# Optimization experiments

Hardware: AMD Instinct MI355X
Metric: run time of the kernel (lower is better)

## Reference

```python
import jax, jax.numpy as jnp
import numpy as np

N_NODES = 50000
N_EDGES = 800000
D_IN = 128
D_HID = 128
D_OUT = 128
EPS = 0.1  # GINConv eps


def setup_inputs() -> dict:
    key = jax.random.key(0)
    k = jax.random.split(key, 8)
    scale = 1.0 / np.sqrt(D_IN)
    return {
        "x": jax.random.normal(k[0], (N_NODES, D_IN), dtype=jnp.float32),
        "edge_index": jax.random.randint(k[1], (2, N_EDGES), 0, N_NODES, dtype=jnp.int64),
        "edge_weight": jax.random.uniform(k[2], (N_EDGES,), dtype=jnp.float32),
        "W1a": jax.random.normal(k[3], (D_IN, D_HID), dtype=jnp.float32) * scale,
        "W1b": jax.random.normal(k[4], (D_HID, D_HID), dtype=jnpp.float32) if False else jax.random.normal(k[4], (D_HID, D_HID), dtype=jnp.float32) * scale,
        "W2a": jax.random.normal(k[5], (D_HID, D_HID), dtype=jnp.float32) * scale,
        "W2b": jax.random.normal(k[6], (D_HID, D_OUT), dtype=jnp.float32) * scale,
    }


def _gin_conv(h, src, dst, ew, Wa, Wb, n_nodes):
    # edge-weighted neighbor sum: aggr[i] = sum_{(j->i)} w_ji * h[j]
    msg = ew[:, None] * h[src]                       # [E, d]
    aggr = jax.ops.segment_sum(msg, dst, num_segments=n_nodes)  # [N, d]
    z = (1.0 + EPS) * h + aggr                       # GIN update
    # 2-layer bias-free MLP: lin -> relu -> lin
    return jnp.maximum(z @ Wa, 0.0) @ Wb


def reference(x, edge_index, edge_weight, W1a, W1b, W2a, W2b):
    src, dst = edge_index[0], edge_index[1]
    n = x.shape[0]
    h = _gin_conv(x, src, dst, edge_weight, W1a, W1b, n)
    h = jnp.maximum(h, 0.0)  # relu between convs; dropout is identity in eval
    h = _gin_conv(h, src, dst, edge_weight, W2a, W2b, n)
    return h
```

## Files before the change

kernel.cpp:

```cpp
#include <hip/hip_runtime.h>
#include <hip/hip_fp16.h>

#define D 128
#define N_NODES 50000
#define EPSP1 1.1f

#define NPB 256
#define NBUCK 196
#define CAP 5120
#define P1E 2048
#define TS 136

typedef __attribute__((ext_vector_type(8))) short short8;
typedef __attribute__((ext_vector_type(4))) float f32x4;

__device__ __forceinline__ unsigned short f2bf(float f) {
    unsigned u = __float_as_uint(f);
    u += 0x7FFF + ((u >> 16) & 1);
    return (unsigned short)(u >> 16);
}
__device__ __forceinline__ float bf2f(unsigned short h) {
    return __uint_as_float(((unsigned)h) << 16);
}

__global__ __launch_bounds__(256) void fused_pre(
    const int* __restrict__ src, const int* __restrict__ dst,
    const float* __restrict__ ew, int* __restrict__ gcnt,
    uint2* __restrict__ gstage, int ne,
    const float* __restrict__ x, unsigned short* __restrict__ hb, int n4,
    const float* __restrict__ W1a, const float* __restrict__ W1b,
    const float* __restrict__ W2a, const float* __restrict__ W2b,
    unsigned short* __restrict__ wp, int p1grid, int cgrid)
{
    int bid = blockIdx.x;
    int tid = threadIdx.x;
    if (bid < p1grid) {
        __shared__ int bcnt[NBUCK];
        __shared__ int goff[NBUCK];
        if (tid < NBUCK) bcnt[tid] = 0;
        __syncthreads();
        int e0 = bid * P1E;
        int   rank[8];
        int   buck[8];
        uint2 pay[8];
#pragma unroll
        for (int j = 0; j < 8; ++j) {
            int e = e0 + j * 256 + tid;
            buck[j] = -1;
            if (e < ne) {
                int d_ = dst[e];
                int b  = d_ >> 8;
                int dl = d_ & 255;
                pay[j].x = (unsigned)(src[e] & 0xFFFF) | ((unsigned)dl << 16);
                pay[j].y = (unsigned)__half_as_ushort(__float2half_rn(ew[e]));
                rank[j]  = atomicAdd(&bcnt[b], 1);
                buck[j]  = b;
            }
        }
        __syncthreads();
        if (tid < NBUCK && bcnt[tid] > 0)
            goff[tid] = atomicAdd(&gcnt[tid], bcnt[tid]);
        __syncthreads();
#pragma unroll
        for (int j = 0; j < 8; ++j) {
            if (buck[j] >= 0) {
                int pos = goff[buck[j]] + rank[j];
                if (pos < CAP)
                    gstage[(size_t)buck[j] * CAP + pos] = pay[j];
            }
        }
    } else if (bid < p1grid + cgrid) {
        int base = (bid - p1grid) * 1024;
#pragma unroll
        for (int it = 0; it < 4; ++it) {
            int i = base + it * 256 + tid;
            if (i < n4) {
                float4 v = ((const float4*)x)[i];
                ushort4 o;
                o.x = f2bf(v.x); o.y = f2bf(v.y); o.z = f2bf(v.z); o.w = f2bf(v.w);
                ((ushort4*)hb)[i] = o;
            }
        }
    } else {
        int pb = bid - p1grid - cgrid;
        int mat = pb >> 3;
        const float* W = (mat == 0) ? W1a : (mat == 1) ? W1b : (mat == 2) ? W2a : W2b;
        unsigned short* Wp = wp + (size_t)mat * 16384;
        int e = (pb & 7) * 256 + tid;
        int col = e & 127;
        int kq  = e >> 7;
        short8 v;
#pragma unroll
        for (int j = 0; j < 8; ++j)
            v[j] = (short)f2bf(W[(size_t)(kq * 8 + j) * 128 + col]);
        ((short8*)Wp)[e] = v;
    }
}

__global__ __launch_bounds__(512) void csr_build(
    const uint2* __restrict__ gstage, const int* __restrict__ gcnt,
    unsigned* __restrict__ epay, int* __restrict__ off)
{
    __shared__ int hist[NPB];
    __shared__ int scan[NPB];
    __shared__ int bscan[NPB];
    __shared__ int loc[NPB];
    __shared__ unsigned csr[CAP];

    int b = blockIdx.x;
    int t = threadIdx.x;
    int cnt = min(gcnt[b], CAP);

    if (t < NPB) hist[t] = 0;
    __syncthreads();

    uint2 ent[CAP / 512];
#pragma unroll
    for (int it = 0; it < CAP / 512; ++it) {
        int i = it * 512 + t;
        if (i < cnt) {
            ent[it] = gstage[(size_t)b * CAP + i];
            atomicAdd(&hist[(ent[it].x >> 16) & 255], 1);
        }
    }
    __syncthreads();

    if (t < NPB) {
        scan[t]  = hist[t];
        bscan[t] = (t < b) ? min(gcnt[t], CAP) : 0;
    }
    __syncthreads();
    for (int dd = 1; dd < NPB; dd <<= 1) {
        int a0 = 0, a1 = 0;
        if (t < NPB && t >= dd) { a0 = scan[t - dd]; a1 = bscan[t - dd]; }
        __syncthreads();
        if (t < NPB && t >= dd) { scan[t] += a0; bscan[t] += a1; }
        __syncthreads();
    }
    int base = bscan[NPB - 1];

    if (t < NPB) {
        int node = (b << 8) + t;
        int excl = scan[t] - hist[t];
        if (node <= N_NODES) off[node] = base + excl;
        loc[t] = excl;
    }
    __syncthreads();

#pragma unroll
    for (int it = 0; it < CAP / 512; ++it) {
        int i = it * 512 + t;
        if (i < cnt) {
            int dl = (ent[it].x >> 16) & 255;
            int p = atomicAdd(&loc[dl], 1);
            csr[p] = (ent[it].x & 0xFFFF) | (ent[it].y << 16);
        }
    }
    __syncthreads();

    for (int i = t; i < cnt; i += 512)
        epay[base + i] = csr[i];
}

__global__ __launch_bounds__(256) void gather_kernel(
    const unsigned short* __restrict__ h, const int* __restrict__ off,
    const unsigned* __restrict__ epay, unsigned short* __restrict__ z, int n_nodes)
{
    int tid = threadIdx.x;
    int node = blockIdx.x * 4 + (tid >> 6);
    if (node >= n_nodes) return;
    int lane = tid & 63;
    int qtr  = lane >> 4;
    int sub  = lane & 15;
    int beg = off[node];
    int end = off[node + 1];
    float acc[8];
#pragma unroll
    for (int c = 0; c < 8; ++c) acc[c] = 0.f;

    int i = beg;
    for (; i + 8 <= end; i += 8) {
        unsigned p0 = epay[i + qtr];
        unsigned p1 = epay[i + 4 + qtr];
        short8 v0 = ((const short8*)(h + (size_t)(p0 & 0xFFFF) * D))[sub];
        short8 v1 = ((const short8*)(h + (size_t)(p1 & 0xFFFF) * D))[sub];
        float w0 = __half2float(__ushort_as_half((unsigned short)(p0 >> 16)));
        float w1 = __half2float(__ushort_as_half((unsigned short)(p1 >> 16)));
#pragma unroll
        for (int c = 0; c < 8; ++c)
            acc[c] += w0 * bf2f((unsigned short)v0[c]) + w1 * bf2f((unsigned short)v1[c]);
    }
    for (; i + qtr < end; i += 4) {
        unsigned p0 = epay[i + qtr];
        short8 v0 = ((const short8*)(h + (size_t)(p0 & 0xFFFF) * D))[sub];
        float w0 = __half2float(__ushort_as_half((unsigned short)(p0 >> 16)));
#pragma unroll
        for (int c = 0; c < 8; ++c)
            acc[c] += w0 * bf2f((unsigned short)v0[c]);
    }

#pragma unroll
    for (int c = 0; c < 8; ++c) {
        acc[c] += __shfl(acc[c], (lane + 32) & 63, 64);
        acc[c] += __shfl(acc[c], (lane + 16) & 63, 64);
    }

    if (qtr == 0) {
        short8 xv = ((const short8*)(h + (size_t)node * D))[sub];
        short8 o;
#pragma unroll
        for (int c = 0; c < 8; ++c) {
            float v = acc[c] + EPSP1 * bf2f((unsigned short)xv[c]);
            o[c] = (short)f2bf(v);
        }
        ((short8*)(z + (size_t)node * D))[sub] = o;
    }
}

template<int RELU2, int OUT_F32>
__global__ __launch_bounds__(256) void mlp_fused(
    const unsigned short* __restrict__ A,
    const unsigned short* __restrict__ WpA,
    const unsigned short* __restrict__ WpB,
    void* __restrict__ outv, int n)
{
    __shared__ unsigned short t[128 * TS];

    int tid  = threadIdx.x;
    int wave = tid >> 6;
    int lane = tid & 63;
    int quad = lane >> 4;
    int lc   = lane & 15;
    int rbase = blockIdx.x * 128 + wave * 32;
    int rloc  = wave * 32;

    const short8 zero8 = {0, 0, 0, 0, 0, 0, 0, 0};

    short8 a[2][4];
#pragma unroll
    for (int s = 0; s < 2; ++s) {
        int row = rbase + s * 16 + lc;
        const unsigned short* ap = A + (size_t)row * D;
#pragma unroll
        for (int kk = 0; kk < 4; ++kk)
            a[s][kk] = (row < n) ? *(const short8*)(ap + kk * 32 + quad * 8) : zero8;
    }

    f32x4 acc[2][8];
#pragma unroll
    for (int s = 0; s < 2; ++s)
#pragma unroll
        for (int c = 0; c < 8; ++c)
            acc[s][c] = (f32x4){0.f, 0.f, 0.f, 0.f};

#pragma unroll
    for (int cf = 0; cf < 8; ++cf) {
        short8 b[4];
#pragma unroll
        for (int kk = 0; kk < 4; ++kk)
            b[kk] = *(const short8*)(WpA + ((size_t)(kk * 4 + quad) * 128 + cf * 16 + lc) * 8);
#pragma unroll
        for (int kk = 0; kk < 4; ++kk) {
            acc[0][cf] = __builtin_amdgcn_mfma_f32_16x16x32_bf16(a[0][kk], b[kk], acc[0][cf], 0, 0, 0);
            acc[1][cf] = __builtin_amdgcn_mfma_f32_16x16x32_bf16(a[1][kk], b[kk], acc[1][cf], 0, 0, 0);
        }
    }

#pragma unroll
    for (int s = 0; s < 2; ++s)
#pragma unroll
        for (int reg = 0; reg < 4; ++reg) {
            int row = rloc + s * 16 + quad * 4 + reg;
#pragma unroll
            for (int cf = 0; cf < 8; ++cf)
                t[row * TS + cf * 16 + lc] = f2bf(fmaxf(acc[s][cf][reg], 0.f));
        }
    __syncthreads();

#pragma unroll
    for (int s = 0; s < 2; ++s) {
        int row = rloc + s * 16 + lc;
#pragma unroll
        for (int kk = 0; kk < 4; ++kk)
            a[s][kk] = *(const short8*)&t[row * TS + kk * 32 + quad * 8];
    }
#pragma unroll
    for (int s = 0; s < 2; ++s)
#pragma unroll
        for (int c = 0; c < 8; ++c)
            acc[s][c] = (f32x4){0.f, 0.f, 0.f, 0.f};

#pragma unroll
    for (int cf = 0; cf < 8; ++cf) {
        short8 b[4];
#pragma unroll
        for (int kk = 0; kk < 4; ++kk)
            b[kk] = *(const short8*)(WpB + ((size_t)(kk * 4 + quad) * 128 + cf * 16 + lc) * 8);
#pragma unroll
        for (int kk = 0; kk < 4; ++kk) {
            acc[0][cf] = __builtin_amdgcn_mfma_f32_16x16x32_bf16(a[0][kk], b[kk], acc[0][cf], 0, 0, 0);
            acc[1][cf] = __builtin_amdgcn_mfma_f32_16x16x32_bf16(a[1][kk], b[kk], acc[1][cf], 0, 0, 0);
        }
    }

#pragma unroll
    for (int s = 0; s < 2; ++s)
#pragma unroll
        for (int reg = 0; reg < 4; ++reg) {
            int row = rbase + s * 16 + quad * 4 + reg;
            if (row < n) {
#pragma unroll
                for (int cf = 0; cf < 8; ++cf) {
                    float v = acc[s][cf][reg];
                    if (RELU2) v = fmaxf(v, 0.f);
                    int col = cf * 16 + lc;
                    if (OUT_F32)
                        ((float*)outv)[(size_t)row * D + col] = v;
                    else
                        ((unsigned short*)outv)[(size_t)row * D + col] = f2bf(v);
                }
            }
        }
}

extern "C" void kernel_launch(void* const* d_in, const int* in_sizes, int n_in,
                              void* d_out, int out_size, void* d_ws, size_t ws_size,
                              hipStream_t stream) {
    const float* x   = (const float*)d_in[0];
    const int*   ei  = (const int*)d_in[1];
    const float* ew  = (const float*)d_in[2];
    const float* W1a = (const float*)d_in[3];
    const float* W1b = (const float*)d_in[4];
    const float* W2a = (const float*)d_in[5];
    const float* W2b = (const float*)d_in[6];
    float* out = (float*)d_out;

    int n_edges = in_sizes[2];
    const int* src = ei;
    const int* dst = ei + n_edges;

    size_t node_elems = (size_t)N_NODES * D;
    unsigned short* hb = (unsigned short*)d_ws;
    unsigned short* zb = hb + node_elems;
    unsigned short* wp = zb + node_elems;
    unsigned* epay = (unsigned*)(wp + 4 * 16384);
    uint2*  gstage = (uint2*)(epay + n_edges);
    int*    gcnt   = (int*)(gstage + (size_t)NBUCK * CAP);
    int*    off    = gcnt + NBUCK;

    int p1grid = (n_edges + P1E - 1) / P1E;
    int cgrid  = ((int)(node_elems / 4) + 1023) / 1024;
    int ggrid  = (N_NODES + 127) / 128;
    int agrid  = (N_NODES + 3) / 4;

    hipMemsetAsync(gcnt, 0, NBUCK * sizeof(int), stream);

    fused_pre<<<p1grid + cgrid + 32, 256, 0, stream>>>(
        src, dst, ew, gcnt, gstage, n_edges,
        x, hb, (int)(node_elems / 4),
        W1a, W1b, W2a, W2b, wp, p1grid, cgrid);

    csr_build<<<NBUCK, 512, 0, stream>>>(gstage, gcnt, epay, off);

    unsigned short* wp0 = wp;
    unsigned short* wp1 = wp + 16384;
    unsigned short* wp2 = wp + 2 * 16384;
    unsigned short* wp3 = wp + 3 * 16384;

    gather_kernel<<<agrid, 256, 0, stream>>>(hb, off, epay, zb, N_NODES);
    mlp_fused<1, 0><<<ggrid, 256, 0, stream>>>(zb, wp0, wp1, hb, N_NODES);

    gather_kernel<<<agrid, 256, 0, stream>>>(hb, off, epay, zb, N_NODES);
    mlp_fused<0, 1><<<ggrid, 256, 0, stream>>>(zb, wp2, wp3, out, N_NODES);
}
```

Before: 201.5 us.

## Move conversions into CSR build kernel, use wave-shuffle scans, unroll gather by 16

Splits edge bucketing into its own kernel and fuses the x and weight bf16 conversions into the CSR-build launch, so the CSR blocks run alongside the conversion blocks instead of the bucketing blocks. The 256-wide shared-memory Hillis-Steele scan with many barriers is replaced by wave-level shuffle scans plus a single-wave reduction for the bucket base offset. The gather loop gains a 16-edge unrolled stage to keep more loads in flight. The grid size hardcodes 782 conversion blocks, which ties the kernel to this node count.

```diff
diff --git a/kernel.cpp b/kernel.cpp
--- a/kernel.cpp
+++ b/kernel.cpp
@@ -23,57 +23,135 @@
     return __uint_as_float(((unsigned)h) << 16);
 }
 
-__global__ __launch_bounds__(256) void fused_pre(
+__global__ __launch_bounds__(256) void pass1_bucket(
     const int* __restrict__ src, const int* __restrict__ dst,
     const float* __restrict__ ew, int* __restrict__ gcnt,
-    uint2* __restrict__ gstage, int ne,
+    uint2* __restrict__ gstage, int ne)
+{
+    __shared__ int bcnt[NBUCK];
+    __shared__ int goff[NBUCK];
+    int tid = threadIdx.x;
+    int bid = blockIdx.x;
+    if (tid < NBUCK) bcnt[tid] = 0;
+    __syncthreads();
+    int e0 = bid * P1E;
+    int   rank[8];
+    int   buck[8];
+    uint2 pay[8];
+#pragma unroll
+    for (int j = 0; j < 8; ++j) {
+        int e = e0 + j * 256 + tid;
+        buck[j] = -1;
+        if (e < ne) {
+            int d_ = dst[e];
+            int b  = d_ >> 8;
+            int dl = d_ & 255;
+            pay[j].x = (unsigned)(src[e] & 0xFFFF) | ((unsigned)dl << 16);
+            pay[j].y = (unsigned)__half_as_ushort(__float2half_rn(ew[e]));
+            rank[j]  = atomicAdd(&bcnt[b], 1);
+            buck[j]  = b;
+        }
+    }
+    __syncthreads();
+    if (tid < NBUCK && bcnt[tid] > 0)
+        goff[tid] = atomicAdd(&gcnt[tid], bcnt[tid]);
+    __syncthreads();
+#pragma unroll
+    for (int j = 0; j < 8; ++j) {
+        if (buck[j] >= 0) {
+            int pos = goff[buck[j]] + rank[j];
+            if (pos < CAP)
+                gstage[(size_t)buck[j] * CAP + pos] = pay[j];
+        }
+    }
+}
+
+__global__ __launch_bounds__(512) void fused_mid(
+    const uint2* __restrict__ gstage, const int* __restrict__ gcnt,
+    unsigned* __restrict__ epay, int* __restrict__ off,
     const float* __restrict__ x, unsigned short* __restrict__ hb, int n4,
     const float* __restrict__ W1a, const float* __restrict__ W1b,
     const float* __restrict__ W2a, const float* __restrict__ W2b,
-    unsigned short* __restrict__ wp, int p1grid, int cgrid)
+    unsigned short* __restrict__ wp)
 {
+    __shared__ int hist[NPB];
+    __shared__ int scn[NPB];
+    __shared__ int loc[NPB];
+    __shared__ int wtot[8];
+    __shared__ int base_s;
+    __shared__ unsigned csr[CAP];
+
     int bid = blockIdx.x;
-    int tid = threadIdx.x;
-    if (bid < p1grid) {
-        __shared__ int bcnt[NBUCK];
-        __shared__ int goff[NBUCK];
-        if (tid < NBUCK) bcnt[tid] = 0;
+    int t = threadIdx.x;
+
+    if (bid < NBUCK) {
+        int b = bid;
+        int cnt = min(gcnt[b], CAP);
+
+        if (t < NPB) hist[t] = 0;
         __syncthreads();
-        int e0 = bid * P1E;
-        int   rank[8];
-        int   buck[8];
-        uint2 pay[8];
-#pragma unroll
-        for (int j = 0; j < 8; ++j) {
-            int e = e0 + j * 256 + tid;
-            buck[j] = -1;
-            if (e < ne) {
-                int d_ = dst[e];
-                int b  = d_ >> 8;
-                int dl = d_ & 255;
-                pay[j].x = (unsigned)(src[e] & 0xFFFF) | ((unsigned)dl << 16);
-                pay[j].y = (unsigned)__half_as_ushort(__float2half_rn(ew[e]));
-                rank[j]  = atomicAdd(&bcnt[b], 1);
-                buck[j]  = b;
+
+        uint2 ent[CAP / 512];
+#pragma unroll
+        for (int it = 0; it < CAP / 512; ++it) {
+            int i = it * 512 + t;
+            if (i < cnt) {
+                ent[it] = gstage[(size_t)b * CAP + i];
+                atomicAdd(&hist[(ent[it].x >> 16) & 255], 1);
             }
         }
         __syncthreads();
-        if (tid < NBUCK && bcnt[tid] > 0)
-            goff[tid] = atomicAdd(&gcnt[tid], bcnt[tid]);
+
+        int w = t >> 6, l = t & 63;
+        if (w < 4) {
+            int v = hist[w * 64 + l];
+#pragma unroll
+            for (int dd = 1; dd < 64; dd <<= 1) {
+                int u = __shfl_up(v, dd, 64);
+                if (l >= dd) v += u;
+            }
+            scn[w * 64 + l] = v;
+            if (l == 63) wtot[w] = v;
+        } else if (w == 4) {
+            int v = 0;
+            for (int i = l; i < NBUCK; i += 64)
+                if (i < b) v += min(gcnt[i], CAP);
+#pragma unroll
+            for (int dd = 32; dd > 0; dd >>= 1) v += __shfl_down(v, dd, 64);
+            if (l == 0) base_s = v;
+        }
         __syncthreads();
-#pragma unroll
-        for (int j = 0; j < 8; ++j) {
-            if (buck[j] >= 0) {
-                int pos = goff[buck[j]] + rank[j];
-                if (pos < CAP)
-                    gstage[(size_t)buck[j] * CAP + pos] = pay[j];
+
+        if (t < NPB) {
+            int pre = 0;
+#pragma unroll
+            for (int j = 0; j < 3; ++j) if (j < w) pre += wtot[j];
+            int incl = scn[t] + pre;
+            int excl = incl - hist[t];
+            int node = (b << 8) + t;
+            if (node <= N_NODES) off[node] = base_s + excl;
+            loc[t] = excl;
+        }
+        __syncthreads();
+
+#pragma unroll
+        for (int it = 0; it < CAP / 512; ++it) {
+            int i = it * 512 + t;
+            if (i < cnt) {
+                int dl = (ent[it].x >> 16) & 255;
+                int p = atomicAdd(&loc[dl], 1);
+                csr[p] = (ent[it].x & 0xFFFF) | (ent[it].y << 16);
             }
         }
-    } else if (bid < p1grid + cgrid) {
-        int base = (bid - p1grid) * 1024;
+        __syncthreads();
+
+        for (int i = t; i < cnt; i += 512)
+            epay[base_s + i] = csr[i];
+    } else if (bid < NBUCK + 782) {
+        int base = (bid - NBUCK) * 2048;
 #pragma unroll
         for (int it = 0; it < 4; ++it) {
-            int i = base + it * 256 + tid;
+            int i = base + it * 512 + t;
             if (i < n4) {
                 float4 v = ((const float4*)x)[i];
                 ushort4 o;
@@ -82,11 +160,11 @@
             }
         }
     } else {
-        int pb = bid - p1grid - cgrid;
-        int mat = pb >> 3;
+        int e2 = (bid - NBUCK - 782) * 512 + t;
+        int mat = e2 >> 11;
+        int e   = e2 & 2047;
         const float* W = (mat == 0) ? W1a : (mat == 1) ? W1b : (mat == 2) ? W2a : W2b;
         unsigned short* Wp = wp + (size_t)mat * 16384;
-        int e = (pb & 7) * 256 + tid;
         int col = e & 127;
         int kq  = e >> 7;
         short8 v;
@@ -95,71 +173,6 @@
             v[j] = (short)f2bf(W[(size_t)(kq * 8 + j) * 128 + col]);
         ((short8*)Wp)[e] = v;
     }
-}
-
-__global__ __launch_bounds__(512) void csr_build(
-    const uint2* __restrict__ gstage, const int* __restrict__ gcnt,
-    unsigned* __restrict__ epay, int* __restrict__ off)
-{
-    __shared__ int hist[NPB];
-    __shared__ int scan[NPB];
-    __shared__ int bscan[NPB];
-    __shared__ int loc[NPB];
-    __shared__ unsigned csr[CAP];
-
-    int b = blockIdx.x;
-    int t = threadIdx.x;
-    int cnt = min(gcnt[b], CAP);
-
-    if (t < NPB) hist[t] = 0;
-    __syncthreads();
-
-    uint2 ent[CAP / 512];
-#pragma unroll
-    for (int it = 0; it < CAP / 512; ++it) {
-        int i = it * 512 + t;
-        if (i < cnt) {
-            ent[it] = gstage[(size_t)b * CAP + i];
-            atomicAdd(&hist[(ent[it].x >> 16) & 255], 1);
-        }
-    }
-    __syncthreads();
-
-    if (t < NPB) {
-        scan[t]  = hist[t];
-        bscan[t] = (t < b) ? min(gcnt[t], CAP) : 0;
-    }
-    __syncthreads();
-    for (int dd = 1; dd < NPB; dd <<= 1) {
-        int a0 = 0, a1 = 0;
-        if (t < NPB && t >= dd) { a0 = scan[t - dd]; a1 = bscan[t - dd]; }
-        __syncthreads();
-        if (t < NPB && t >= dd) { scan[t] += a0; bscan[t] += a1; }
-        __syncthreads();
-    }
-    int base = bscan[NPB - 1];
-
-    if (t < NPB) {
-        int node = (b << 8) + t;
-        int excl = scan[t] - hist[t];
-        if (node <= N_NODES) off[node] = base + excl;
-        loc[t] = excl;
-    }
-    __syncthreads();
-
-#pragma unroll
-    for (int it = 0; it < CAP / 512; ++it) {
-        int i = it * 512 + t;
-        if (i < cnt) {
-            int dl = (ent[it].x >> 16) & 255;
-            int p = atomicAdd(&loc[dl], 1);
-            csr[p] = (ent[it].x & 0xFFFF) | (ent[it].y << 16);
-        }
-    }
-    __syncthreads();
-
-    for (int i = t; i < cnt; i += 512)
-        epay[base + i] = csr[i];
 }
 
 __global__ __launch_bounds__(256) void gather_kernel(
@@ -179,6 +192,24 @@
     for (int c = 0; c < 8; ++c) acc[c] = 0.f;
 
     int i = beg;
+    for (; i + 16 <= end; i += 16) {
+        unsigned p0 = epay[i + qtr];
+        unsigned p1 = epay[i + 4 + qtr];
+        unsigned p2 = epay[i + 8 + qtr];
+        unsigned p3 = epay[i + 12 + qtr];
+        short8 v0 = ((const short8*)(h + (size_t)(p0 & 0xFFFF) * D))[sub];
+        short8 v1 = ((const short8*)(h + (size_t)(p1 & 0xFFFF) * D))[sub];
+        short8 v2 = ((const short8*)(h + (size_t)(p2 & 0xFFFF) * D))[sub];
+        short8 v3 = ((const short8*)(h + (size_t)(p3 & 0xFFFF) * D))[sub];
+        float w0 = __half2float(__ushort_as_half((unsigned short)(p0 >> 16)));
+        float w1 = __half2float(__ushort_as_half((unsigned short)(p1 >> 16)));
+        float w2 = __half2float(__ushort_as_half((unsigned short)(p2 >> 16)));
+        float w3 = __half2float(__ushort_as_half((unsigned short)(p3 >> 16)));
+#pragma unroll
+        for (int c = 0; c < 8; ++c)
+            acc[c] += w0 * bf2f((unsigned short)v0[c]) + w1 * bf2f((unsigned short)v1[c])
+                    + w2 * bf2f((unsigned short)v2[c]) + w3 * bf2f((unsigned short)v3[c]);
+    }
     for (; i + 8 <= end; i += 8) {
         unsigned p0 = epay[i + qtr];
         unsigned p1 = epay[i + 4 + qtr];
@@ -349,18 +380,17 @@
     int*    off    = gcnt + NBUCK;
 
     int p1grid = (n_edges + P1E - 1) / P1E;
-    int cgrid  = ((int)(node_elems / 4) + 1023) / 1024;
     int ggrid  = (N_NODES + 127) / 128;
     int agrid  = (N_NODES + 3) / 4;
+    int n4     = (int)(node_elems / 4);
 
     hipMemsetAsync(gcnt, 0, NBUCK * sizeof(int), stream);
 
-    fused_pre<<<p1grid + cgrid + 32, 256, 0, stream>>>(
-        src, dst, ew, gcnt, gstage, n_edges,
-        x, hb, (int)(node_elems / 4),
-        W1a, W1b, W2a, W2b, wp, p1grid, cgrid);
-
-    csr_build<<<NBUCK, 512, 0, stream>>>(gstage, gcnt, epay, off);
+    pass1_bucket<<<p1grid, 256, 0, stream>>>(src, dst, ew, gcnt, gstage, n_edges);
+
+    fused_mid<<<NBUCK + 782 + 16, 512, 0, stream>>>(
+        gstage, gcnt, epay, off,
+        x, hb, n4, W1a, W1b, W2a, W2b, wp);
 
     unsigned short* wp0 = wp;
     unsigned short* wp1 = wp + 16384;
```

Result: no change. 201.4 us (-0.1%).
